# Performance work log

Measured on AMD Instinct MI355X. Metric: run time of the kernel, lower is better.

Reference implementation:

```python
import jax, jax.numpy as jnp
import numpy as np

NUM_SAMPLES = 9


def _resize1d(x, out_size, axis):
    """Bilinear (align_corners=False) resize along one axis, matching torch."""
    in_size = x.shape[axis]
    scale = in_size / out_size
    dst = jnp.arange(out_size, dtype=jnp.float32)
    src = jnp.maximum((dst + 0.5) * scale - 0.5, 0.0)
    i0 = jnp.floor(src).astype(jnp.int32)
    w1 = (src - i0).astype(x.dtype)
    i0 = jnp.clip(i0, 0, in_size - 1)
    i1 = jnp.clip(i0 + 1, 0, in_size - 1)
    x0 = jnp.take(x, i0, axis=axis)
    x1 = jnp.take(x, i1, axis=axis)
    wshape = [1] * x.ndim
    wshape[axis] = out_size
    w1 = w1.reshape(wshape)
    return x0 * (1.0 - w1) + x1 * w1


def _rel_to_abs(x, ns):
    # x: (b, h, l, ns+l-1) -> (b, h, l, ns) via the pad/reshape skew trick
    b, h, l, c = x.shape
    x = jnp.pad(x, ((0, 0), (0, 0), (0, 0), (0, 1)))
    x = x.reshape(b, h, l * (c + 1))
    x = jnp.pad(x, ((0, 0), (0, 0), (0, ns - 1)))
    x = x.reshape(b, h, l + 1, ns + l - 1)
    return x[:, :, :l, l - 1:]


def _relative_logits_1d(q, rel_k, ns):
    # q: (b, heads, x, y, d); rel_k: (y+ns-1, d)
    logits = jnp.einsum('bhxyd,rd->bhxyr', q, rel_k)
    b, h, x, y, r = logits.shape
    logits = logits.reshape(b, h * x, y, r)
    return _rel_to_abs(logits, ns)


def setup_inputs() -> dict:
    key = jax.random.key(0)
    k1, k2, k3 = jax.random.split(key, 3)
    B, heads, Hh, Ww, d = 16, 8, 64, 64, 64
    scale = d ** (-0.5)
    q = jax.random.normal(k1, (B, heads, Hh, Ww, d), dtype=jnp.float32)
    rel_height = jax.random.normal(k2, (Hh + NUM_SAMPLES - 1, d), dtype=jnp.float32) * scale
    rel_width = jax.random.normal(k3, (Ww + NUM_SAMPLES - 1, d), dtype=jnp.float32) * scale
    return {"q": q, "H": Hh, "W": Ww, "rel_height": rel_height, "rel_width": rel_width}


def reference(q, H, W, rel_height, rel_width):
    ns = NUM_SAMPLES
    heads = q.shape[1]
    # bilinear resize of learned tables along the positional axis
    # (the dim_head axis is resized to its own size -> identity)
    rel_w = _resize1d(rel_width, W + ns - 1, axis=0)
    rel_h = _resize1d(rel_height, H + ns - 1, axis=0)

    rel_logits_w = _relative_logits_1d(q, rel_w, ns)          # (b, heads*H, W, ns)
    qT = jnp.swapaxes(q, 2, 3)                                # (b, heads, W, H, d)
    rel_logits_h = _relative_logits_1d(qT, rel_h, ns)         # (b, heads*W, H, ns)

    # torch interpolates (b, ns, heads*W, H) -> (heads*H, W); separable bilinear
    rel_logits_h = _resize1d(rel_logits_h, heads * H, axis=1)
    rel_logits_h = _resize1d(rel_logits_h, W, axis=2)
    return rel_logits_w + rel_logits_h
```

## Files before the change

kernel.cpp:

```cpp
#include <hip/hip_runtime.h>
#include <stdint.h>

#define NS 9

typedef _Float16 f16x8 __attribute__((ext_vector_type(8)));
typedef float    f32x4 __attribute__((ext_vector_type(4)));

#define SBAR __builtin_amdgcn_sched_barrier(0)
#define WAIT_VM(N) do { SBAR; asm volatile("s_waitcnt vmcnt(" #N ")" ::: "memory"); SBAR; } while (0)
#define WAIT_LGKM(N) do { SBAR; asm volatile("s_waitcnt lgkmcnt(" #N ")" ::: "memory"); SBAR; } while (0)

__device__ __forceinline__ unsigned int pk(float a, float b) {
    return __builtin_bit_cast(unsigned int, __builtin_amdgcn_cvt_pkrtz(a, b));
}


__global__ __launch_bounds__(512, 4) void relpos_kernel(
    const float* __restrict__ q,
    const float* __restrict__ relh,
    const float* __restrict__ relw,
    float* __restrict__ out)
{
    __shared__ uint4 S1[16][16][8];
    __shared__ uint4 S2[16][16][8];
    __shared__ uint4 RL[2][2][32][8];

    const int blk = blockIdx.x;
    const int bh  = blk & 127;
    const int wid = blk >> 7;
    const int ta  = wid < 4 ? 0 : wid < 7 ? 1 : wid < 9 ? 2 : 3;
    const int tc  = wid < 4 ? wid : wid < 7 ? wid - 3 : wid < 9 ? wid - 5 : 3;
    const int Ta0 = ta << 4, Tc0 = tc << 4;

    const int t    = threadIdx.x;
    const int lane = t & 63;
    const int wvu  = __builtin_amdgcn_readfirstlane(t >> 6);
    const int wg   = wvu >> 2;
    const int wl   = wvu & 3;
    const int jl   = lane & 15;
    const int k4p  = lane >> 4;

    const float* __restrict__ qs = q + ((size_t)bh << 18);

    float4 sA[8], sB[8], sR[3];
#pragma unroll
    for (int i = 0; i < 8; ++i) {
        const int F  = (i << 9) + t;
        const int al = F >> 8, cc = (F >> 4) & 15, g = F & 15;
        sA[i] = *(const float4*)(qs + (size_t)(Ta0 + al) * 4096
                                    + (size_t)(Tc0 + cc) * 64 + (g << 2));
    }
    SBAR;
#pragma unroll
    for (int i = 0; i < 8; ++i) {
        const int F  = (i << 9) + t;
        const int al = F >> 8, cc = (F >> 4) & 15, g = F & 15;
        sB[i] = *(const float4*)(qs + (size_t)(Tc0 + al) * 4096
                                    + (size_t)(Ta0 + cc) * 64 + (g << 2));
    }
    SBAR;
#pragma unroll
    for (int m = 0; m < 3; ++m) {
        const int F   = (m << 9) + t;
        const int win = F >= 768;
        const int r   = F - (win ? 768 : 0);
        const int tbl = r >= 384;
        const int rr  = r - (tbl ? 384 : 0);
        const int row = rr >> 4, g = rr & 15;
        const int rb0 = win ? (48 - Ta0) : (48 - Tc0);
        int gr = rb0 + row; if (gr > 71) gr = 71;
        sR[m] = *(const float4*)((tbl ? relw : relh) + (size_t)gr * 64 + (g << 2));
    }
    SBAR;

    WAIT_VM(11);
#pragma unroll
    for (int i = 0; i < 8; ++i) {
        const int F  = (i << 9) + t;
        const int al = F >> 8, cc = (F >> 4) & 15, g = F & 15;
        const int slot = (g >> 1) ^ ((al ^ cc) & 7), half = g & 1;
        uint2 w; w.x = pk(sA[i].x, sA[i].y); w.y = pk(sA[i].z, sA[i].w);
        ((uint2*)&S1[al][cc][slot])[half] = w;
    }
    WAIT_VM(3);
#pragma unroll
    for (int i = 0; i < 8; ++i) {
        const int F  = (i << 9) + t;
        const int al = F >> 8, cc = (F >> 4) & 15, g = F & 15;
        const int slot = (g >> 1) ^ ((al ^ cc) & 7), half = g & 1;
        uint2 w; w.x = pk(sB[i].x, sB[i].y); w.y = pk(sB[i].z, sB[i].w);
        ((uint2*)&S2[al][cc][slot])[half] = w;
    }
    WAIT_VM(0);
#pragma unroll
    for (int m = 0; m < 3; ++m) {
        const int F   = (m << 9) + t;
        const int win = F >= 768;
        const int r   = F - (win ? 768 : 0);
        const int tbl = r >= 384;
        const int rr  = r - (tbl ? 384 : 0);
        const int row = rr >> 4, g = rr & 15;
        const int slot = (g >> 1) ^ (row & 7), half = g & 1;
        uint2 w; w.x = pk(sR[m].x, sR[m].y); w.y = pk(sR[m].z, sR[m].w);
        ((uint2*)&RL[win][tbl][row][slot])[half] = w;
    }
    WAIT_LGKM(0);
    __builtin_amdgcn_s_barrier();

    if (wg == 0 || ta != tc) {
        const uint4 (*P)[16][8] = wg ? S2 : S1;
        const uint4 (*Q)[16][8] = wg ? S1 : S2;
        const int win   = wg;
        const int Arow0 = wg ? Tc0 : Ta0;
        const int Ccol0 = wg ? Ta0 : Tc0;

        uint4 A0[4], B0[4], A1[4], B1[4];
        auto RD = [&](int r, uint4* A, uint4* B) {
            const int kh = (r & 1) << 2;
#pragma unroll
            for (int it = 0; it < 4; ++it) {
                const int cl = (wl << 2) | it;
                const int sx = (jl ^ cl) & 7;
                A[it] = (r < 2) ? P[jl][cl][(kh + k4p) ^ sx]
                                : Q[cl][jl][(kh + k4p) ^ sx];
                const int rl = (15 - cl) + jl;
                B[it] = RL[win][r < 2 ? 1 : 0][rl][(kh + k4p) ^ (rl & 7)];
            }
        };
        f32x4 acc[4];
#pragma unroll
        for (int it = 0; it < 4; ++it) acc[it] = (f32x4){0.f, 0.f, 0.f, 0.f};
        auto MF = [&](const uint4* A, const uint4* B) {
#pragma unroll
            for (int it = 0; it < 4; ++it)
                acc[it] = __builtin_amdgcn_mfma_f32_16x16x32_f16(
                    __builtin_bit_cast(f16x8, A[it]),
                    __builtin_bit_cast(f16x8, B[it]), acc[it], 0, 0, 0);
        };
        RD(0, A0, B0); RD(1, A1, B1);
        WAIT_LGKM(8);  MF(A0, B0);  RD(2, A0, B0);
        WAIT_LGKM(8);  MF(A1, B1);  RD(3, A1, B1);
        WAIT_LGKM(8);  MF(A0, B0);
        WAIT_LGKM(0);  MF(A1, B1);

        if (jl < NS) {
            const int ar = k4p << 2;
            const size_t ob = (size_t)bh << 6;
#pragma unroll
            for (int it = 0; it < 4; ++it) {
                const int cl = (wl << 2) | it;
#pragma unroll
                for (int r = 0; r < 4; ++r)
                    out[((ob + (Arow0 + ar + r)) * 64 + (Ccol0 + cl)) * NS + jl] = acc[it][r];
            }
        }
    }
}

extern "C" void kernel_launch(void* const* d_in, const int* in_sizes, int n_in,
                              void* d_out, int out_size, void* d_ws, size_t ws_size,
                              hipStream_t stream) {
    const float* q    = (const float*)d_in[0];
    const float* relh = (const float*)d_in[3];
    const float* relw = (const float*)d_in[4];
    float* out = (float*)d_out;

    relpos_kernel<<<dim3(1280), dim3(512), 0, stream>>>(q, relh, relw, out);
}
```

Measured before the change: 31.19 us.

## Make blocks persistent over multiple tile units with prefetch of the next unit

The grid shrinks from 1280 to 512 blocks, and each block now loops over 2–3 tile units (wid = w0 + 4u). The global loads for the next unit are issued right after the current unit's data is written to LDS, so the loads overlap that unit's MFMA compute and stores. Launch bounds are relaxed to 2 blocks per SIMD to allow more registers for the prefetched data. The cost is fewer resident waves, extra barriers, and uneven work per block, since some blocks take 3 units and others 2.

```diff
diff --git a/kernel.cpp b/kernel.cpp
--- a/kernel.cpp
+++ b/kernel.cpp
@@ -15,7 +15,7 @@
 }
 
 
-__global__ __launch_bounds__(512, 4) void relpos_kernel(
+__global__ __launch_bounds__(512, 2) void relpos_kernel(
     const float* __restrict__ q,
     const float* __restrict__ relh,
     const float* __restrict__ relw,
@@ -25,12 +25,10 @@
     __shared__ uint4 S2[16][16][8];
     __shared__ uint4 RL[2][2][32][8];
 
-    const int blk = blockIdx.x;
-    const int bh  = blk & 127;
-    const int wid = blk >> 7;
-    const int ta  = wid < 4 ? 0 : wid < 7 ? 1 : wid < 9 ? 2 : 3;
-    const int tc  = wid < 4 ? wid : wid < 7 ? wid - 3 : wid < 9 ? wid - 5 : 3;
-    const int Ta0 = ta << 4, Tc0 = tc << 4;
+    const int b   = blockIdx.x;
+    const int bh  = b & 127;
+    const int w0  = b >> 7;
+    const int nu  = (w0 < 2) ? 3 : 2;
 
     const int t    = threadIdx.x;
     const int lane = t & 63;
@@ -42,72 +40,78 @@
 
     const float* __restrict__ qs = q + ((size_t)bh << 18);
 
+    auto TAf = [](int wid) { return (wid < 4 ? 0 : wid < 7 ? 1 : wid < 9 ? 2 : 3) << 4; };
+    auto TCf = [](int wid) { return (wid < 4 ? wid : wid < 7 ? wid - 3 : wid < 9 ? wid - 5 : 3) << 4; };
+
     float4 sA[8], sB[8], sR[3];
+
+    auto issueUnit = [&](int wid) {
+        const int Ta0 = TAf(wid), Tc0 = TCf(wid);
 #pragma unroll
-    for (int i = 0; i < 8; ++i) {
-        const int F  = (i << 9) + t;
-        const int al = F >> 8, cc = (F >> 4) & 15, g = F & 15;
-        sA[i] = *(const float4*)(qs + (size_t)(Ta0 + al) * 4096
-                                    + (size_t)(Tc0 + cc) * 64 + (g << 2));
-    }
-    SBAR;
+        for (int i = 0; i < 8; ++i) {
+            const int F = (i << 9) + t;
+            const int al = F >> 8, cc = (F >> 4) & 15, g = F & 15;
+            sA[i] = *(const float4*)(qs + (size_t)(Ta0 + al) * 4096
+                                        + (size_t)(Tc0 + cc) * 64 + (g << 2));
+        }
+        SBAR;
 #pragma unroll
-    for (int i = 0; i < 8; ++i) {
-        const int F  = (i << 9) + t;
-        const int al = F >> 8, cc = (F >> 4) & 15, g = F & 15;
-        sB[i] = *(const float4*)(qs + (size_t)(Tc0 + al) * 4096
-                                    + (size_t)(Ta0 + cc) * 64 + (g << 2));
-    }
-    SBAR;
+        for (int i = 0; i < 8; ++i) {
+            const int F = (i << 9) + t;
+            const int al = F >> 8, cc = (F >> 4) & 15, g = F & 15;
+            sB[i] = *(const float4*)(qs + (size_t)(Tc0 + al) * 4096
+                                        + (size_t)(Ta0 + cc) * 64 + (g << 2));
+        }
+        SBAR;
 #pragma unroll
-    for (int m = 0; m < 3; ++m) {
-        const int F   = (m << 9) + t;
-        const int win = F >= 768;
-        const int r   = F - (win ? 768 : 0);
-        const int tbl = r >= 384;
-        const int rr  = r - (tbl ? 384 : 0);
-        const int row = rr >> 4, g = rr & 15;
-        const int rb0 = win ? (48 - Ta0) : (48 - Tc0);
-        int gr = rb0 + row; if (gr > 71) gr = 71;
-        sR[m] = *(const float4*)((tbl ? relw : relh) + (size_t)gr * 64 + (g << 2));
-    }
-    SBAR;
+        for (int m = 0; m < 3; ++m) {
+            const int F = (m << 9) + t;
+            const int win = F >= 768;
+            const int r = F - (win ? 768 : 0);
+            const int tbl = r >= 384;
+            const int rr = r - (tbl ? 384 : 0);
+            const int row = rr >> 4, g = rr & 15;
+            const int rb0 = win ? (48 - Ta0) : (48 - Tc0);
+            int gr = rb0 + row; if (gr > 71) gr = 71;
+            sR[m] = *(const float4*)((tbl ? relw : relh) + (size_t)gr * 64 + (g << 2));
+        }
+        SBAR;
+    };
 
-    WAIT_VM(11);
+    auto writeLDS = [&]() {
 #pragma unroll
-    for (int i = 0; i < 8; ++i) {
-        const int F  = (i << 9) + t;
-        const int al = F >> 8, cc = (F >> 4) & 15, g = F & 15;
-        const int slot = (g >> 1) ^ ((al ^ cc) & 7), half = g & 1;
-        uint2 w; w.x = pk(sA[i].x, sA[i].y); w.y = pk(sA[i].z, sA[i].w);
-        ((uint2*)&S1[al][cc][slot])[half] = w;
-    }
-    WAIT_VM(3);
+        for (int i = 0; i < 8; ++i) {
+            const int F = (i << 9) + t;
+            const int al = F >> 8, cc = (F >> 4) & 15, g = F & 15;
+            const int slot = (g >> 1) ^ ((al ^ cc) & 7), half = g & 1;
+            uint2 w; w.x = pk(sA[i].x, sA[i].y); w.y = pk(sA[i].z, sA[i].w);
+            ((uint2*)&S1[al][cc][slot])[half] = w;
+        }
 #pragma unroll
-    for (int i = 0; i < 8; ++i) {
-        const int F  = (i << 9) + t;
-        const int al = F >> 8, cc = (F >> 4) & 15, g = F & 15;
-        const int slot = (g >> 1) ^ ((al ^ cc) & 7), half = g & 1;
-        uint2 w; w.x = pk(sB[i].x, sB[i].y); w.y = pk(sB[i].z, sB[i].w);
-        ((uint2*)&S2[al][cc][slot])[half] = w;
-    }
-    WAIT_VM(0);
+        for (int i = 0; i < 8; ++i) {
+            const int F = (i << 9) + t;
+            const int al = F >> 8, cc = (F >> 4) & 15, g = F & 15;
+            const int slot = (g >> 1) ^ ((al ^ cc) & 7), half = g & 1;
+            uint2 w; w.x = pk(sB[i].x, sB[i].y); w.y = pk(sB[i].z, sB[i].w);
+            ((uint2*)&S2[al][cc][slot])[half] = w;
+        }
 #pragma unroll
-    for (int m = 0; m < 3; ++m) {
-        const int F   = (m << 9) + t;
-        const int win = F >= 768;
-        const int r   = F - (win ? 768 : 0);
-        const int tbl = r >= 384;
-        const int rr  = r - (tbl ? 384 : 0);
-        const int row = rr >> 4, g = rr & 15;
-        const int slot = (g >> 1) ^ (row & 7), half = g & 1;
-        uint2 w; w.x = pk(sR[m].x, sR[m].y); w.y = pk(sR[m].z, sR[m].w);
-        ((uint2*)&RL[win][tbl][row][slot])[half] = w;
-    }
-    WAIT_LGKM(0);
-    __builtin_amdgcn_s_barrier();
+        for (int m = 0; m < 3; ++m) {
+            const int F = (m << 9) + t;
+            const int win = F >= 768;
+            const int r = F - (win ? 768 : 0);
+            const int tbl = r >= 384;
+            const int rr = r - (tbl ? 384 : 0);
+            const int row = rr >> 4, g = rr & 15;
+            const int slot = (g >> 1) ^ (row & 7), half = g & 1;
+            uint2 w; w.x = pk(sR[m].x, sR[m].y); w.y = pk(sR[m].z, sR[m].w);
+            ((uint2*)&RL[win][tbl][row][slot])[half] = w;
+        }
+    };
 
-    if (wg == 0 || ta != tc) {
+    auto computeStore = [&](int wid) {
+        const int Ta0 = TAf(wid), Tc0 = TCf(wid);
+        if (wg == 1 && Ta0 == Tc0) return;
         const uint4 (*P)[16][8] = wg ? S2 : S1;
         const uint4 (*Q)[16][8] = wg ? S1 : S2;
         const int win   = wg;
@@ -154,6 +158,18 @@
                     out[((ob + (Arow0 + ar + r)) * 64 + (Ccol0 + cl)) * NS + jl] = acc[it][r];
             }
         }
+    };
+
+    issueUnit(w0);
+    for (int u = 0; u < nu; ++u) {
+        const int wid = w0 + 4 * u;
+        if (u > 0) __builtin_amdgcn_s_barrier();
+        WAIT_VM(0);
+        writeLDS();
+        if (u + 1 < nu) issueUnit(w0 + 4 * (u + 1));
+        WAIT_LGKM(0);
+        __builtin_amdgcn_s_barrier();
+        computeStore(wid);
     }
 }
 
@@ -165,5 +181,5 @@
     const float* relw = (const float*)d_in[4];
     float* out = (float*)d_out;
 
-    relpos_kernel<<<dim3(1280), dim3(512), 0, stream>>>(q, relh, relw, out);
+    relpos_kernel<<<dim3(512), dim3(512), 0, stream>>>(q, relh, relw, out);
 }
```

Result: slower. 34.34 us (+10.1%).
